# Optimization experiments

Hardware: AMD Instinct MI355X
Metric: run time of the kernel (lower is better)

## Reference

```python
import jax, jax.numpy as jnp
import numpy as np

D_MODEL = 1024
NUM_HEADS = 16
D_K = D_MODEL // NUM_HEADS
B, T = 2, 2048


def setup_inputs() -> dict:
    key = jax.random.key(0)
    ks = jax.random.split(key, 9)
    s = 1.0 / np.sqrt(D_MODEL)
    inp = {"x": jax.random.normal(ks[0], (B, T, D_MODEL), dtype=jnp.float32)}
    for i, name in enumerate(["q", "k", "v", "out"]):
        inp[f"W_{name}"] = jax.random.uniform(ks[1 + 2 * i], (D_MODEL, D_MODEL), jnp.float32, -s, s)
        inp[f"b_{name}"] = jax.random.uniform(ks[2 + 2 * i], (D_MODEL,), jnp.float32, -s, s)
    return inp


def reference(x, W_q, b_q, W_k, b_k, W_v, b_v, W_out, b_out):
    b, t, _ = x.shape
    # torch Linear: y = x @ W.T + b
    def proj(inp, W, bias):
        y = inp @ W.T + bias
        return y.reshape(b, -1, NUM_HEADS, D_K).transpose(0, 2, 1, 3)  # [B,H,T,d_k]

    Q = proj(x, W_q, b_q)
    K = proj(x, W_k, b_k)
    V = proj(x, W_v, b_v)
    scores = jnp.einsum("bhqd,bhkd->bhqk", Q, K) / jnp.sqrt(jnp.float32(D_K))
    attn = jax.nn.softmax(scores, axis=-1)
    ctx = jnp.einsum("bhqk,bhkd->bhqd", attn, V)
    ctx = ctx.transpose(0, 2, 1, 3).reshape(b, t, D_MODEL)
    return ctx @ W_out.T + b_out
```

## Files before the change

kernel.cpp:

```cpp
#include <hip/hip_runtime.h>
#include <hip/hip_bf16.h>

typedef __attribute__((ext_vector_type(8))) short short8;
typedef __attribute__((ext_vector_type(4))) short short4v;
typedef __attribute__((ext_vector_type(4))) float floatx4;

__device__ __forceinline__ unsigned short f2b(float f) {
  unsigned int v;
  __builtin_memcpy(&v, &f, 4);
  unsigned int r = (v + 0x7FFFu + ((v >> 16) & 1u)) >> 16;
  return (unsigned short)r;
}

__device__ __forceinline__ unsigned int f2b_pk(float a, float b) {
#if __has_builtin(__builtin_amdgcn_cvt_pk_bf16_f32)
  typedef __attribute__((ext_vector_type(2))) __bf16 bf16x2;
  bf16x2 r = __builtin_amdgcn_cvt_pk_bf16_f32(a, b);
  unsigned int u;
  __builtin_memcpy(&u, &r, 4);
  return u;
#else
  return ((unsigned int)f2b(b) << 16) | (unsigned int)f2b(a);
#endif
}

__device__ __forceinline__ float fast_exp2(float x) {
#if __has_builtin(__builtin_amdgcn_exp2f)
  return __builtin_amdgcn_exp2f(x);
#else
  return __builtin_exp2f(x);
#endif
}

__device__ __forceinline__ void async_copy16(const void* g, void* l) {
  __builtin_amdgcn_global_load_lds(
      (const __attribute__((address_space(1))) unsigned int*)g,
      (__attribute__((address_space(3))) unsigned int*)l, 16, 0, 0);
}

#define QSCALE 0.18033688011112042f


__global__ __launch_bounds__(256) void cvt_all_kernel(
    const float* __restrict__ x,
    const float* __restrict__ w0, const float* __restrict__ w1,
    const float* __restrict__ w2, const float* __restrict__ w3,
    unsigned short* __restrict__ xb,
    unsigned short* __restrict__ d0, unsigned short* __restrict__ d1,
    unsigned short* __restrict__ d2, unsigned short* __restrict__ d3)
{
  int gid = blockIdx.x * 256 + threadIdx.x;
  const float* src;
  unsigned short* dst;
  size_t off;
  if (gid < (1 << 20)) {
    src = x; dst = xb; off = gid;
  } else {
    int g = gid - (1 << 20);
    int w = g >> 18;
    off = g & 0x3FFFF;
    src = (w == 0) ? w0 : (w == 1) ? w1 : (w == 2) ? w2 : w3;
    dst = (w == 0) ? d0 : (w == 1) ? d1 : (w == 2) ? d2 : d3;
  }
  floatx4 v = *(const floatx4*)(src + off * 4);
  unsigned int lo = f2b_pk(v[0], v[1]), hi = f2b_pk(v[2], v[3]);
  unsigned long long r = ((unsigned long long)hi << 32) | lo;
  *(unsigned long long*)(dst + off * 4) = r;
}

__global__ __launch_bounds__(256) void gemm_qkv_kernel(
    const unsigned short* __restrict__ A,
    const unsigned short* __restrict__ W0, const unsigned short* __restrict__ W1,
    const unsigned short* __restrict__ W2,
    const float* __restrict__ bias0, const float* __restrict__ bias1,
    const float* __restrict__ bias2,
    unsigned short* __restrict__ Qo, unsigned short* __restrict__ Ko,
    unsigned short* __restrict__ VTo)
{
  const int z = blockIdx.z;
  const unsigned short* W  = (z == 0) ? W0 : (z == 1) ? W1 : W2;
  const float* bias        = (z == 0) ? bias0 : (z == 1) ? bias1 : bias2;

  __shared__ alignas(16) unsigned short sA[128 * 32];
  __shared__ alignas(16) unsigned short sB[128 * 32];

  const int tid  = threadIdx.x;
  const int lane = tid & 63;
  const int wave = tid >> 6;
  const int col  = lane & 15;
  const int quad = lane >> 4;
  const int wm   = (wave >> 1) * 64;
  const int wn   = (wave & 1) * 64;
  const int m0   = blockIdx.y * 128;
  const int n0   = blockIdx.x * 128;
  const int swz8 = (quad ^ ((col >> 1) & 3)) * 8;

  floatx4 acc[4][4];
#pragma unroll
  for (int i = 0; i < 4; ++i)
#pragma unroll
    for (int j = 0; j < 4; ++j) acc[i][j] = (floatx4){0.f, 0.f, 0.f, 0.f};

  for (int k0 = 0; k0 < 1024; k0 += 32) {
    __syncthreads();
#pragma unroll
    for (int i = 0; i < 2; ++i) {
      int c   = i * 256 + tid;
      int row = c >> 2;
      int cs  = (c & 3) ^ ((c >> 3) & 3);
      int ko  = cs * 8;
      async_copy16(A + (size_t)(m0 + row) * 1024 + k0 + ko, sA + c * 8);
      async_copy16(W + (size_t)(n0 + row) * 1024 + k0 + ko, sB + c * 8);
    }
    __syncthreads();
    short8 af[4], bf[4];
#pragma unroll
    for (int mi = 0; mi < 4; ++mi)
      af[mi] = *(const short8*)(sA + (wm + mi * 16 + col) * 32 + swz8);
#pragma unroll
    for (int ni = 0; ni < 4; ++ni)
      bf[ni] = *(const short8*)(sB + (wn + ni * 16 + col) * 32 + swz8);
#pragma unroll
    for (int mi = 0; mi < 4; ++mi)
#pragma unroll
      for (int ni = 0; ni < 4; ++ni)
        acc[mi][ni] = __builtin_amdgcn_mfma_f32_16x16x32_bf16(af[mi], bf[ni], acc[mi][ni], 0, 0, 0);
  }

#pragma unroll
  for (int ni = 0; ni < 4; ++ni) {
    int n = n0 + wn + ni * 16 + col;
    float bv = bias[n];
#pragma unroll
    for (int mi = 0; mi < 4; ++mi) {
      int mbase = m0 + wm + mi * 16 + quad * 4;
#pragma unroll
      for (int r = 0; r < 4; ++r) {
        int m = mbase + r;
        float val = acc[mi][ni][r] + bv;
        if (z == 0) {
          Qo[(size_t)m * 1024 + n] = f2b(val * QSCALE);
        } else if (z == 1) {
          Ko[(size_t)m * 1024 + n] = f2b(val);
        } else {
          int d = n & 63, h = n >> 6;
          int bb = m >> 11, t = m & 2047;
          VTo[(((size_t)bb * 16 + h) * 64 + d) * 2048 + t] = f2b(val);
        }
      }
    }
  }
}

__global__ __launch_bounds__(256) void gemm_out_kernel(
    const unsigned short* __restrict__ A, const unsigned short* __restrict__ W,
    const float* __restrict__ bias, float* __restrict__ DF)
{
  __shared__ alignas(16) unsigned short sA[128 * 32];
  __shared__ alignas(16) unsigned short sB[64 * 32];

  const int tid  = threadIdx.x;
  const int lane = tid & 63;
  const int wave = tid >> 6;
  const int col  = lane & 15;
  const int quad = lane >> 4;
  const int wm   = (wave >> 1) * 64;
  const int wn   = (wave & 1) * 32;
  const int m0   = blockIdx.y * 128;
  const int n0   = blockIdx.x * 64;
  const int swz8 = (quad ^ ((col >> 1) & 3)) * 8;

  floatx4 acc[4][2];
#pragma unroll
  for (int i = 0; i < 4; ++i)
#pragma unroll
    for (int j = 0; j < 2; ++j) acc[i][j] = (floatx4){0.f, 0.f, 0.f, 0.f};

  for (int k0 = 0; k0 < 1024; k0 += 32) {
    __syncthreads();
#pragma unroll
    for (int i = 0; i < 2; ++i) {
      int c   = i * 256 + tid;
      int row = c >> 2;
      int cs  = (c & 3) ^ ((c >> 3) & 3);
      async_copy16(A + (size_t)(m0 + row) * 1024 + k0 + cs * 8, sA + c * 8);
    }
    {
      int row = tid >> 2;
      int cs  = (tid & 3) ^ ((tid >> 3) & 3);
      async_copy16(W + (size_t)(n0 + row) * 1024 + k0 + cs * 8, sB + tid * 8);
    }
    __syncthreads();
    short8 af[4], bf[2];
#pragma unroll
    for (int mi = 0; mi < 4; ++mi)
      af[mi] = *(const short8*)(sA + (wm + mi * 16 + col) * 32 + swz8);
#pragma unroll
    for (int ni = 0; ni < 2; ++ni)
      bf[ni] = *(const short8*)(sB + (wn + ni * 16 + col) * 32 + swz8);
#pragma unroll
    for (int mi = 0; mi < 4; ++mi)
#pragma unroll
      for (int ni = 0; ni < 2; ++ni)
        acc[mi][ni] = __builtin_amdgcn_mfma_f32_16x16x32_bf16(af[mi], bf[ni], acc[mi][ni], 0, 0, 0);
  }

#pragma unroll
  for (int ni = 0; ni < 2; ++ni) {
    int n = n0 + wn + ni * 16 + col;
    float bv = bias[n];
#pragma unroll
    for (int mi = 0; mi < 4; ++mi) {
      int mbase = m0 + wm + mi * 16 + quad * 4;
#pragma unroll
      for (int r = 0; r < 4; ++r)
        DF[(size_t)(mbase + r) * 1024 + n] = acc[mi][ni][r] + bv;
    }
  }
}

__global__ __launch_bounds__(256, 4) void attention_kernel(
    const unsigned short* __restrict__ Q, const unsigned short* __restrict__ K,
    const unsigned short* __restrict__ VT, unsigned short* __restrict__ CTX)
{
  __shared__ alignas(16) unsigned short sQ[2 * 64 * 32];
  __shared__ alignas(16) unsigned short sK[2 * 64 * 32];
  __shared__ alignas(16) unsigned short sV[2 * 64 * 32];
  __shared__ alignas(16) unsigned short sP[4][16 * 72];

  const int bh = blockIdx.x;
  const int b = bh >> 4, h = bh & 15;
  const int q0 = blockIdx.y * 64;
  const int tid  = threadIdx.x;
  const int lane = tid & 63;
  const int wave = tid >> 6;
  const int col  = lane & 15;
  const int quad = lane >> 4;
  const int swz8 = (quad ^ ((col >> 1) & 3)) * 8;

  const int srow = tid >> 2;
  const int sko  = ((tid & 3) ^ ((tid >> 3) & 3)) * 8;

#pragma unroll
  for (int i = 0; i < 2; ++i) {
    async_copy16(Q + (size_t)(b * 2048 + q0 + srow) * 1024 + h * 64 + i * 32 + sko,
                 sQ + (i * 256 + tid) * 8);
  }
  __syncthreads();
  short8 qf[2];
  qf[0] = *(const short8*)(sQ + (wave * 16 + col) * 32 + swz8);
  qf[1] = *(const short8*)(sQ + 2048 + (wave * 16 + col) * 32 + swz8);

  floatx4 Oacc[4];
#pragma unroll
  for (int f = 0; f < 4; ++f) Oacc[f] = (floatx4){0.f, 0.f, 0.f, 0.f};
  float lacc = 0.f;

  unsigned short* myP = &sP[wave][0];

  for (int kt = 0; kt < 2048; kt += 64) {
    __syncthreads();
#pragma unroll
    for (int i = 0; i < 2; ++i) {
      async_copy16(K + (size_t)(b * 2048 + kt + srow) * 1024 + h * 64 + i * 32 + sko,
                   sK + (i * 256 + tid) * 8);
      async_copy16(VT + ((size_t)bh * 64 + srow) * 2048 + kt + i * 32 + sko,
                   sV + (i * 256 + tid) * 8);
    }
    __syncthreads();

    floatx4 ST[4];
#pragma unroll
    for (int f = 0; f < 4; ++f) {
      ST[f] = (floatx4){0.f, 0.f, 0.f, 0.f};
      short8 kf0 = *(const short8*)(sK + (f * 16 + col) * 32 + swz8);
      ST[f] = __builtin_amdgcn_mfma_f32_16x16x32_bf16(kf0, qf[0], ST[f], 0, 0, 0);
      short8 kf1 = *(const short8*)(sK + 2048 + (f * 16 + col) * 32 + swz8);
      ST[f] = __builtin_amdgcn_mfma_f32_16x16x32_bf16(kf1, qf[1], ST[f], 0, 0, 0);
    }

#pragma unroll
    for (int f = 0; f < 4; ++f) {
      float p0 = fast_exp2(ST[f][0]);
      float p1 = fast_exp2(ST[f][1]);
      float p2 = fast_exp2(ST[f][2]);
      float p3 = fast_exp2(ST[f][3]);
      lacc += (p0 + p1) + (p2 + p3);
      unsigned long long w =
          ((unsigned long long)f2b_pk(p2, p3) << 32) | f2b_pk(p0, p1);
      *(unsigned long long*)(myP + col * 72 + f * 16 + quad * 4) = w;
    }

    short8 pf0 = *(const short8*)(myP + col * 72 + quad * 8);
    short8 pf1 = *(const short8*)(myP + col * 72 + 32 + quad * 8);
#pragma unroll
    for (int f = 0; f < 4; ++f) {
      short8 vf0 = *(const short8*)(sV + (f * 16 + col) * 32 + swz8);
      Oacc[f] = __builtin_amdgcn_mfma_f32_16x16x32_bf16(pf0, vf0, Oacc[f], 0, 0, 0);
      short8 vf1 = *(const short8*)(sV + 2048 + (f * 16 + col) * 32 + swz8);
      Oacc[f] = __builtin_amdgcn_mfma_f32_16x16x32_bf16(pf1, vf1, Oacc[f], 0, 0, 0);
    }
  }

  lacc += __shfl_xor(lacc, 16, 64);
  lacc += __shfl_xor(lacc, 32, 64);
  float inv[4];
#pragma unroll
  for (int r = 0; r < 4; ++r) inv[r] = 1.f / __shfl(lacc, quad * 4 + r, 16);

#pragma unroll
  for (int f = 0; f < 4; ++f) {
#pragma unroll
    for (int r = 0; r < 4; ++r) {
      int q = q0 + wave * 16 + quad * 4 + r;
      int d = f * 16 + col;
      CTX[(size_t)(b * 2048 + q) * 1024 + h * 64 + d] = f2b(Oacc[f][r] * inv[r]);
    }
  }
}

extern "C" void kernel_launch(void* const* d_in, const int* in_sizes, int n_in,
                              void* d_out, int out_size, void* d_ws, size_t ws_size,
                              hipStream_t stream) {
  const float* x   = (const float*)d_in[0];
  const float* W_q = (const float*)d_in[1];
  const float* b_q = (const float*)d_in[2];
  const float* W_k = (const float*)d_in[3];
  const float* b_k = (const float*)d_in[4];
  const float* W_v = (const float*)d_in[5];
  const float* b_v = (const float*)d_in[6];
  const float* W_o = (const float*)d_in[7];
  const float* b_o = (const float*)d_in[8];
  float* out = (float*)d_out;

  const size_t NX = (size_t)4096 * 1024;
  const size_t NW = (size_t)1024 * 1024;

  unsigned short* p   = (unsigned short*)d_ws;
  unsigned short* xb  = p;  p += NX;
  unsigned short* Wqb = p;  p += NW;
  unsigned short* Wkb = p;  p += NW;
  unsigned short* Wvb = p;  p += NW;
  unsigned short* Wob = p;  p += NW;
  unsigned short* Q   = p;  p += NX;
  unsigned short* Kb  = p;  p += NX;
  unsigned short* VT  = p;  p += NX;
  unsigned short* CTX = p;  p += NX;

  dim3 blk(256);
  cvt_all_kernel<<<dim3(8192), blk, 0, stream>>>(
      x, W_q, W_k, W_v, W_o, xb, Wqb, Wkb, Wvb, Wob);
  gemm_qkv_kernel<<<dim3(8, 32, 3), blk, 0, stream>>>(
      xb, Wqb, Wkb, Wvb, b_q, b_k, b_v, Q, Kb, VT);
  attention_kernel<<<dim3(32, 32), blk, 0, stream>>>(Q, Kb, VT, CTX);
  gemm_out_kernel<<<dim3(16, 32), blk, 0, stream>>>(CTX, Wob, b_o, out);
}
```

Measured before the change: 202.1 us.

## Keep attention probabilities in registers by computing transposed O, dropping LDS P round-trip

Computes the output tile transposed (V^T as the A operand, P as B) so the exp'd score fragments from the S^T MFMA are already in the register layout needed for the PV MFMA. This removes the per-wave shared-memory P buffer along with its stores and reloads. V fragments are now gathered as two 4-element swizzled LDS reads, the row-sum normalization uses the lane-local sum, and the output is written as packed 64-bit stores. Occupancy hint raised to 6 blocks per CU, which the smaller LDS footprint allows but which may force register pressure.

```diff
diff --git a/kernel.cpp b/kernel.cpp
--- a/kernel.cpp
+++ b/kernel.cpp
@@ -219,14 +219,13 @@
   }
 }
 
-__global__ __launch_bounds__(256, 4) void attention_kernel(
+__global__ __launch_bounds__(256, 6) void attention_kernel(
     const unsigned short* __restrict__ Q, const unsigned short* __restrict__ K,
     const unsigned short* __restrict__ VT, unsigned short* __restrict__ CTX)
 {
   __shared__ alignas(16) unsigned short sQ[2 * 64 * 32];
   __shared__ alignas(16) unsigned short sK[2 * 64 * 32];
   __shared__ alignas(16) unsigned short sV[2 * 64 * 32];
-  __shared__ alignas(16) unsigned short sP[4][16 * 72];
 
   const int bh = blockIdx.x;
   const int b = bh >> 4, h = bh & 15;
@@ -251,12 +250,14 @@
   qf[0] = *(const short8*)(sQ + (wave * 16 + col) * 32 + swz8);
   qf[1] = *(const short8*)(sQ + 2048 + (wave * 16 + col) * 32 + swz8);
 
+  const int vsw  = (col >> 1) & 3;
+  const int vch0 = ((quad >> 1) ^ vsw) * 8 + (quad & 1) * 4;
+  const int vch1 = (((quad >> 1) | 2) ^ vsw) * 8 + (quad & 1) * 4;
+
   floatx4 Oacc[4];
 #pragma unroll
-  for (int f = 0; f < 4; ++f) Oacc[f] = (floatx4){0.f, 0.f, 0.f, 0.f};
+  for (int nd = 0; nd < 4; ++nd) Oacc[nd] = (floatx4){0.f, 0.f, 0.f, 0.f};
   float lacc = 0.f;
-
-  unsigned short* myP = &sP[wave][0];
 
   for (int kt = 0; kt < 2048; kt += 64) {
     __syncthreads();
@@ -279,42 +280,49 @@
       ST[f] = __builtin_amdgcn_mfma_f32_16x16x32_bf16(kf1, qf[1], ST[f], 0, 0, 0);
     }
 
-#pragma unroll
-    for (int f = 0; f < 4; ++f) {
-      float p0 = fast_exp2(ST[f][0]);
-      float p1 = fast_exp2(ST[f][1]);
-      float p2 = fast_exp2(ST[f][2]);
-      float p3 = fast_exp2(ST[f][3]);
-      lacc += (p0 + p1) + (p2 + p3);
-      unsigned long long w =
-          ((unsigned long long)f2b_pk(p2, p3) << 32) | f2b_pk(p0, p1);
-      *(unsigned long long*)(myP + col * 72 + f * 16 + quad * 4) = w;
-    }
-
-    short8 pf0 = *(const short8*)(myP + col * 72 + quad * 8);
-    short8 pf1 = *(const short8*)(myP + col * 72 + 32 + quad * 8);
-#pragma unroll
-    for (int f = 0; f < 4; ++f) {
-      short8 vf0 = *(const short8*)(sV + (f * 16 + col) * 32 + swz8);
-      Oacc[f] = __builtin_amdgcn_mfma_f32_16x16x32_bf16(pf0, vf0, Oacc[f], 0, 0, 0);
-      short8 vf1 = *(const short8*)(sV + 2048 + (f * 16 + col) * 32 + swz8);
-      Oacc[f] = __builtin_amdgcn_mfma_f32_16x16x32_bf16(pf1, vf1, Oacc[f], 0, 0, 0);
+    short8 pf[2];
+#pragma unroll
+    for (int s = 0; s < 2; ++s) {
+      float p00 = fast_exp2(ST[2 * s][0]);
+      float p01 = fast_exp2(ST[2 * s][1]);
+      float p02 = fast_exp2(ST[2 * s][2]);
+      float p03 = fast_exp2(ST[2 * s][3]);
+      float p10 = fast_exp2(ST[2 * s + 1][0]);
+      float p11 = fast_exp2(ST[2 * s + 1][1]);
+      float p12 = fast_exp2(ST[2 * s + 1][2]);
+      float p13 = fast_exp2(ST[2 * s + 1][3]);
+      lacc += ((p00 + p01) + (p02 + p03)) + ((p10 + p11) + (p12 + p13));
+      alignas(16) unsigned int d4[4] = {
+          f2b_pk(p00, p01), f2b_pk(p02, p03), f2b_pk(p10, p11), f2b_pk(p12, p13)};
+      __builtin_memcpy(&pf[s], d4, 16);
+    }
+
+#pragma unroll
+    for (int s = 0; s < 2; ++s) {
+#pragma unroll
+      for (int nd = 0; nd < 4; ++nd) {
+        const unsigned short* vrow = sV + s * 2048 + (nd * 16 + col) * 32;
+        short4v v0 = *(const short4v*)(vrow + vch0);
+        short4v v1 = *(const short4v*)(vrow + vch1);
+        short8 vf = (short8){v0[0], v0[1], v0[2], v0[3], v1[0], v1[1], v1[2], v1[3]};
+        Oacc[nd] = __builtin_amdgcn_mfma_f32_16x16x32_bf16(vf, pf[s], Oacc[nd], 0, 0, 0);
+      }
     }
   }
 
   lacc += __shfl_xor(lacc, 16, 64);
   lacc += __shfl_xor(lacc, 32, 64);
-  float inv[4];
-#pragma unroll
-  for (int r = 0; r < 4; ++r) inv[r] = 1.f / __shfl(lacc, quad * 4 + r, 16);
-
-#pragma unroll
-  for (int f = 0; f < 4; ++f) {
-#pragma unroll
-    for (int r = 0; r < 4; ++r) {
-      int q = q0 + wave * 16 + quad * 4 + r;
-      int d = f * 16 + col;
-      CTX[(size_t)(b * 2048 + q) * 1024 + h * 64 + d] = f2b(Oacc[f][r] * inv[r]);
+  float inv = 1.f / lacc;
+
+  {
+    int q = q0 + wave * 16 + col;
+    unsigned short* dst = CTX + (size_t)(b * 2048 + q) * 1024 + h * 64;
+#pragma unroll
+    for (int nd = 0; nd < 4; ++nd) {
+      unsigned int lo = f2b_pk(Oacc[nd][0] * inv, Oacc[nd][1] * inv);
+      unsigned int hi = f2b_pk(Oacc[nd][2] * inv, Oacc[nd][3] * inv);
+      unsigned long long w = ((unsigned long long)hi << 32) | lo;
+      *(unsigned long long*)(dst + nd * 16 + quad * 4) = w;
     }
   }
 }
```

Result: no change. 204.9 us (+1.4%).
